# Kernel optimization log

Hardware: AMD Instinct MI355X
Metric: run time of the kernel (lower is better)

Reference implementation:

```python
import jax, jax.numpy as jnp
import numpy as np

NUM_NODES = 40000
NUM_EDGES = 400000
DIM = 128
NUM_REL = 502  # num_relation * 2
NUM_HEAD = 1


def setup_inputs() -> dict:
    key = jax.random.key(0)
    ks = jax.random.split(key, 16)
    d = DIM
    return {
        "curr_stat": jax.random.normal(ks[0], (NUM_NODES, d), jnp.float32),
        "last_stat": jax.random.normal(ks[1], (NUM_NODES, d), jnp.float32),
        "relemb_weight": jax.random.normal(ks[2], (NUM_REL, d), jnp.float32),
        "selfrel_weight": jax.random.normal(ks[3], (1, d), jnp.float32),
        "Wq": jax.random.normal(ks[4], (2 * d, d), jnp.float32) * (1.0 / np.sqrt(2 * d)),
        "bq": jax.random.normal(ks[5], (d,), jnp.float32) * 0.02,
        "Wk": jax.random.normal(ks[6], (2 * d, d), jnp.float32) * (1.0 / np.sqrt(2 * d)),
        "bk": jax.random.normal(ks[7], (d,), jnp.float32) * 0.02,
        "Wv": jax.random.normal(ks[8], (d, d), jnp.float32) * (1.0 / np.sqrt(d)),
        "bv": jax.random.normal(ks[9], (d,), jnp.float32) * 0.02,
        "dyn_weight": jax.random.normal(ks[10], (d, d), jnp.float32) * (1.0 / np.sqrt(d)),
        "edge_index": jax.random.randint(ks[11], (2, NUM_EDGES), 0, NUM_NODES, jnp.int32),
        "edge_type": jax.random.randint(ks[12], (NUM_EDGES,), 0, NUM_REL, jnp.int32),
    }


def _segment_softmax(scores, seg, num_segments):
    # scores: [E, H]; softmax over edges sharing the same destination segment
    m = jax.ops.segment_max(scores, seg, num_segments=num_segments)  # [N, H]
    e = jnp.exp(scores - m[seg])
    s = jax.ops.segment_sum(e, seg, num_segments=num_segments)  # [N, H]
    return e / s[seg]


def reference(curr_stat, last_stat, relemb_weight, selfrel_weight,
              Wq, bq, Wk, bk, Wv, bv, dyn_weight,
              edge_index, edge_type):
    N, D = curr_stat.shape
    H = NUM_HEAD
    HD = D // H

    # append self-loop edges for every node, with the dedicated self-relation
    loop = jnp.arange(N, dtype=edge_index.dtype)
    src = jnp.concatenate([edge_index[0], loop])  # [E_total]
    dst = jnp.concatenate([edge_index[1], loop])  # [E_total]
    type_emb = jnp.concatenate(
        [relemb_weight[edge_type], jnp.broadcast_to(selfrel_weight, (N, D))], axis=0)

    E = src.shape[0]
    # linear projections (x @ W + b); torch Linear stores W transposed, same math
    q = (jnp.concatenate([curr_stat[dst], type_emb], -1) @ Wq + bq).reshape(E, H, HD)
    k = (jnp.concatenate([last_stat[src], type_emb], -1) @ Wk + bk).reshape(E, H, HD)
    v = (last_stat[src] @ Wv + bv).reshape(E, H, HD)

    attn = jnp.sum(q * k, axis=-1) / np.sqrt(HD).astype(np.float32)  # [E, H]

    dyn_prob = _segment_softmax(attn, dst, N)   # [E, H]
    sta_prob = _segment_softmax(-attn, dst, N)  # [E, H]

    counts = jax.ops.segment_sum(jnp.ones((E,), jnp.float32), dst, num_segments=N)
    denom = jnp.maximum(counts, 1.0)[:, None]  # scatter-mean denominator

    feat_dyn = jax.ops.segment_sum((dyn_prob[..., None] * v).reshape(E, D), dst,
                                   num_segments=N) / denom
    feat_sta = jax.ops.segment_sum((sta_prob[..., None] * v).reshape(E, D), dst,
                                   num_segments=N) / denom

    # stack (feat_sta, feat_dyn @ dyn_weight) -> [2, N, D]
    return jnp.stack([feat_sta, feat_dyn @ dyn_weight])
```

## Files before the change

### kernel.cpp

```cpp
#include <hip/hip_runtime.h>
#include <hip/hip_bf16.h>
#include <math.h>

#define DIMC 128
#define CS2L (0.08838834764831845f * 1.4426950408889634f)

typedef __attribute__((ext_vector_type(8))) short short8;
typedef __attribute__((ext_vector_type(4))) float floatx4;
typedef __attribute__((ext_vector_type(2))) float f32x2;

static __device__ __forceinline__ unsigned pk2(float lo, float hi) {
    __hip_bfloat162 h = __float22bfloat162_rn(make_float2(lo, hi));
    return *(unsigned*)&h;
}
static __device__ __forceinline__ unsigned short f2bf(float x) {
    union { float f; unsigned int u; } v; v.f = x;
    unsigned int r = v.u + 0x7FFFu + ((v.u >> 16) & 1u);
    return (unsigned short)(r >> 16);
}
static __device__ __forceinline__ f32x2 bfp(unsigned int u) {
    union { unsigned int i; float f; } a, b;
    a.i = u << 16; b.i = u & 0xFFFF0000u;
    f32x2 r; r.x = a.f; r.y = b.f; return r;
}

template<int CTRL>
static __device__ __forceinline__ float dpp_add(float x) {
    int y = __builtin_amdgcn_update_dpp(0, __float_as_int(x), CTRL, 0xF, 0xF, true);
    return x + __int_as_float(y);
}
static __device__ __forceinline__ float red16(float p) {
    p = dpp_add<0xB1>(p);
    p = dpp_add<0x4E>(p);
    p = dpp_add<0x141>(p);
    p = dpp_add<0x140>(p);
    return p;
}

struct PrepArgs {
    const float* W[6];
    unsigned short* F[6];
    float wscale[6];
    const float* relemb; const float* selfrel;
    float* TypeEmb;
    int* deg;
    int R; int N;
};

__global__ __launch_bounds__(64) void prep_all(PrepArgs a)
{
    int b = blockIdx.x;
    int lane = threadIdx.x;
    if (b < 192) {
        int mat = b >> 5, ts = b & 31;
        int s = ts & 3, t = ts >> 2;
        int q = lane >> 4, c = lane & 15;
        const float* W = a.W[mat];
        float sc = a.wscale[mat];
        unsigned short o[8];
        #pragma unroll
        for (int j = 0; j < 8; ++j)
            o[j] = f2bf(W[(long)(s * 32 + q * 8 + j) * DIMC + t * 16 + c] * sc);
        uint4 u;
        u.x = (unsigned)o[0] | ((unsigned)o[1] << 16);
        u.y = (unsigned)o[2] | ((unsigned)o[3] << 16);
        u.z = (unsigned)o[4] | ((unsigned)o[5] << 16);
        u.w = (unsigned)o[6] | ((unsigned)o[7] << 16);
        ((uint4*)a.F[mat])[ts * 64 + lane] = u;
    } else if (b < 192 + a.R + 1) {
        int r = b - 192;
        const float* src = (r < a.R) ? (a.relemb + (long)r * DIMC) : a.selfrel;
        float2 v = ((const float2*)src)[lane];
        ((float2*)(a.TypeEmb + (long)r * DIMC))[lane] = v;
    } else {
        int i = (b - (192 + a.R + 1)) * 64 + lane;
        if (i < a.N) a.deg[i] = 0;
    }
}

struct GemmM5 {
    const float*          Af[5];
    const unsigned short* Ab[5];
    const unsigned short* F[5];
    const float*          bias[5];
    float                 bscale[5];
    float*                outf[5];
    unsigned short*       outb[5];
    int                   ostride[5];
    int                   ooff[5];
    int                   M[5];
    const unsigned short* F2;
    const float*          bias2;
    unsigned short*       outb2;
    const int*            hist_dst;
    int*                  hist_deg;
    int                   hist_E;
};

__global__ __launch_bounds__(256) void gemm_mfma(GemmM5 g)
{
    __shared__ uint4 wlds[2048];

    if (blockIdx.y == 4) {
        int i = blockIdx.x * blockDim.x + threadIdx.x;
        int stride = gridDim.x * blockDim.x;
        for (; i < g.hist_E; i += stride) atomicAdd(&g.hist_deg[g.hist_dst[i]], 1);
        return;
    }

    const int wave = threadIdx.x >> 6;
    const int lane = threadIdx.x & 63;
    const int q = lane >> 4, c = lane & 15;

    if (blockIdx.y == 1) {
        const int M = g.M[1];
        if ((int)blockIdx.x * 64 >= M) return;
        const int rowbase = blockIdx.x * 64 + wave * 16;

        {
            const uint4* Fp = (const uint4*)g.F[1];
            #pragma unroll
            for (int j = 0; j < 8; ++j)
                wlds[threadIdx.x + j * 256] = Fp[threadIdx.x + j * 256];
        }
        int rowA = rowbase + c; if (rowA > M - 1) rowA = M - 1;
        short8 af[4];
        {
            const float* Ar = g.Af[1] + (long)rowA * DIMC + q * 8;
            #pragma unroll
            for (int s = 0; s < 4; ++s) {
                float4 x0 = *(const float4*)(Ar + s * 32);
                float4 x1 = *(const float4*)(Ar + s * 32 + 4);
                uint4 u;
                u.x = pk2(x0.x, x0.y);
                u.y = pk2(x0.z, x0.w);
                u.z = pk2(x1.x, x1.y);
                u.w = pk2(x1.z, x1.w);
                af[s] = *(short8*)&u;
            }
        }
        floatx4 acc[8];
        #pragma unroll
        for (int t = 0; t < 8; ++t) acc[t] = (floatx4){0.f, 0.f, 0.f, 0.f};
        __syncthreads();
        #pragma unroll
        for (int t = 0; t < 8; ++t)
            #pragma unroll
            for (int s = 0; s < 4; ++s) {
                uint4 u = wlds[(t * 4 + s) * 64 + lane];
                acc[t] = __builtin_amdgcn_mfma_f32_16x16x32_bf16(af[s], *(short8*)&u, acc[t], 0, 0, 0);
            }
        __syncthreads();
        {
            const uint4* Fp = (const uint4*)g.F2;
            #pragma unroll
            for (int j = 0; j < 8; ++j)
                wlds[threadIdx.x + j * 256] = Fp[threadIdx.x + j * 256];
        }
        #pragma unroll
        for (int t = 0; t < 8; ++t)
            #pragma unroll
            for (int r = 0; r < 4; ++r) {
                float other = __shfl_xor(acc[t][r], 1);
                int row = rowbase + q * 4 + r;
                if ((lane & 1) == 0 && row < M)
                    ((unsigned*)g.outb[1])[(long)row * 64 + t * 8 + (c >> 1)] = pk2(acc[t][r], other);
            }
        #pragma unroll
        for (int t = 0; t < 8; ++t) {
            float b = g.bias2[t * 16 + c];
            acc[t] = (floatx4){b, b, b, b};
        }
        __syncthreads();
        #pragma unroll
        for (int t = 0; t < 8; ++t)
            #pragma unroll
            for (int s = 0; s < 4; ++s) {
                uint4 u = wlds[(t * 4 + s) * 64 + lane];
                acc[t] = __builtin_amdgcn_mfma_f32_16x16x32_bf16(af[s], *(short8*)&u, acc[t], 0, 0, 0);
            }
        #pragma unroll
        for (int t = 0; t < 8; ++t)
            #pragma unroll
            for (int r = 0; r < 4; ++r) {
                float other = __shfl_xor(acc[t][r], 1);
                int row = rowbase + q * 4 + r;
                if ((lane & 1) == 0 && row < M)
                    ((unsigned*)g.outb2)[(long)row * 64 + t * 8 + (c >> 1)] = pk2(acc[t][r], other);
            }
        return;
    }

    const int which = blockIdx.y;
    const int M = g.M[which];
    if ((int)blockIdx.x * 64 >= M) return;

    const float*          __restrict__ Af   = g.Af[which];
    const unsigned short* __restrict__ Ab   = g.Ab[which];
    const unsigned short* __restrict__ F    = g.F[which];
    const float*          __restrict__ bias = g.bias[which];
    const float bsc = g.bscale[which];
    float*          __restrict__ outf = g.outf[which];
    unsigned short* __restrict__ outb = g.outb[which];
    const int ostride = g.ostride[which];
    const int ooff    = g.ooff[which];
    const int rowbase = blockIdx.x * 64 + wave * 16;

    {
        const uint4* Fp = (const uint4*)F;
        #pragma unroll
        for (int j = 0; j < 8; ++j)
            wlds[threadIdx.x + j * 256] = Fp[threadIdx.x + j * 256];
    }

    int rowA = rowbase + c; if (rowA > M - 1) rowA = M - 1;
    short8 af[4];
    if (Af) {
        const float* Ar = Af + (long)rowA * DIMC + q * 8;
        #pragma unroll
        for (int s = 0; s < 4; ++s) {
            float4 x0 = *(const float4*)(Ar + s * 32);
            float4 x1 = *(const float4*)(Ar + s * 32 + 4);
            uint4 u;
            u.x = pk2(x0.x, x0.y);
            u.y = pk2(x0.z, x0.w);
            u.z = pk2(x1.x, x1.y);
            u.w = pk2(x1.z, x1.w);
            af[s] = *(short8*)&u;
        }
    } else {
        const unsigned short* Ar = Ab + (long)rowA * DIMC + q * 8;
        #pragma unroll
        for (int s = 0; s < 4; ++s) {
            uint4 u = *(const uint4*)(Ar + s * 32);
            af[s] = *(short8*)&u;
        }
    }

    floatx4 acc[8];
    #pragma unroll
    for (int t = 0; t < 8; ++t) {
        float b = bias ? bias[t * 16 + c] * bsc : 0.0f;
        acc[t] = (floatx4){b, b, b, b};
    }

    __syncthreads();

    #pragma unroll
    for (int t = 0; t < 8; ++t)
        #pragma unroll
        for (int s = 0; s < 4; ++s) {
            uint4 u = wlds[(t * 4 + s) * 64 + lane];
            acc[t] = __builtin_amdgcn_mfma_f32_16x16x32_bf16(af[s], *(short8*)&u, acc[t], 0, 0, 0);
        }

    if (outf) {
        #pragma unroll
        for (int t = 0; t < 8; ++t)
            #pragma unroll
            for (int r = 0; r < 4; ++r) {
                int row = rowbase + q * 4 + r;
                if (row < M)
                    outf[(long)row * DIMC + t * 16 + c] = acc[t][r];
            }
    } else {
        #pragma unroll
        for (int t = 0; t < 8; ++t)
            #pragma unroll
            for (int r = 0; r < 4; ++r) {
                float other = __shfl_xor(acc[t][r], 1);
                int row = rowbase + q * 4 + r;
                if ((lane & 1) == 0 && row < M) {
                    unsigned word = pk2(acc[t][r], other);
                    ((unsigned*)outb)[((long)row * 64 + t * 8 + (c >> 1))
                                      * (long)ostride + ooff] = word;
                }
            }
    }
}

__global__ __launch_bounds__(256) void partial_sums(const int* __restrict__ deg,
                                                    int* __restrict__ partial, int N)
{
    __shared__ int sh[256];
    int t = threadIdx.x;
    int beg = blockIdx.x * 1024 + t * 4;
    int s = 0;
    if (beg + 3 < N) { int4 v = *(const int4*)(deg + beg); s = v.x + v.y + v.z + v.w; }
    else { for (int j = 0; j < 4; ++j) if (beg + j < N) s += deg[beg + j]; }
    sh[t] = s;
    __syncthreads();
    for (int d = 128; d >= 1; d >>= 1) {
        if (t < d) sh[t] += sh[t + d];
        __syncthreads();
    }
    if (t == 0) partial[blockIdx.x] = sh[0];
}

__global__ __launch_bounds__(256) void scan_write_offsets(const int* __restrict__ deg,
                                                          const int* __restrict__ partial,
                                                          int* __restrict__ offs,
                                                          int* __restrict__ cursor, int N, int nb)
{
    __shared__ int sh[256];
    __shared__ int sbase;
    int t = threadIdx.x;
    if (t < 64) {
        int v = (t < nb && t < (int)blockIdx.x) ? partial[t] : 0;
        #pragma unroll
        for (int d = 32; d >= 1; d >>= 1) v += __shfl_xor(v, d);
        if (t == 0) sbase = v;
    }
    int beg = blockIdx.x * 1024 + t * 4;
    int d0 = 0, d1 = 0, d2 = 0, d3 = 0;
    if (beg + 3 < N) { int4 v = *(const int4*)(deg + beg); d0 = v.x; d1 = v.y; d2 = v.z; d3 = v.w; }
    else {
        if (beg < N)     d0 = deg[beg];
        if (beg + 1 < N) d1 = deg[beg + 1];
        if (beg + 2 < N) d2 = deg[beg + 2];
        if (beg + 3 < N) d3 = deg[beg + 3];
    }
    int s = d0 + d1 + d2 + d3;
    sh[t] = s;
    __syncthreads();
    for (int d = 1; d < 256; d <<= 1) {
        int v = (t >= d) ? sh[t - d] : 0;
        __syncthreads();
        sh[t] += v;
        __syncthreads();
    }
    int base = sbase + sh[t] - s;
    int o0 = base, o1 = o0 + d0, o2 = o1 + d1, o3 = o2 + d2;
    if (beg < N)     { offs[beg]     = o0; cursor[beg]     = o0; }
    if (beg + 1 < N) { offs[beg + 1] = o1; cursor[beg + 1] = o1; }
    if (beg + 2 < N) { offs[beg + 2] = o2; cursor[beg + 2] = o2; }
    if (beg + 3 < N) { offs[beg + 3] = o3; cursor[beg + 3] = o3; }
}

__global__ void scatter_kernel(const int* __restrict__ src, const int* __restrict__ dst,
                               const int* __restrict__ etype, int* __restrict__ cursor,
                               int2* __restrict__ sedge, int E)
{
    int e = blockIdx.x * blockDim.x + threadIdx.x;
    if (e < E) {
        int d = dst[e];
        int p = atomicAdd(&cursor[d], 1);
        sedge[p] = make_int2(src[e] << 8, etype[e] << 9);
    }
}

__global__ __launch_bounds__(256) void node_kernel(
    const char*  __restrict__ Qb,
    const char*  __restrict__ Kb,
    const char*  __restrict__ Vb,
    const char*  __restrict__ QKb,
    const int* __restrict__ offs, const int* __restrict__ deg,
    const int2* __restrict__ sedge,
    float* __restrict__ out_sta, uint2* __restrict__ feat_dyn,
    int N, int R)
{
    int n = (blockIdx.x * blockDim.x + threadIdx.x) >> 6;
    int lane = threadIdx.x & 63;
    if (n >= N) return;
    const int ql = lane & 31;
    const int h  = lane >> 5;
    const int lo8  = ql << 3;
    const int lo16 = ql << 4;

    int base = offs[n];
    int dcnt = deg[n];
    int etot = dcnt + 1;

    f32x2 q01, q23;
    {
        uint2 qw = *(const uint2*)(Qb + ((long)n << 8) + lo8);
        q01 = bfp(qw.x);
        q23 = bfp(qw.y);
    }

    float s_d = 0.0f, s_s = 0.0f;
    f32x2 accd0 = {0.f, 0.f}, accd1 = accd0;
    f32x2 accs0 = accd0, accs1 = accd0;

    const int selfK = n << 8, selfQ = R << 9;

    int T = (etot + 1) >> 1;
    for (int it = 0; it < T; ++it) {
        int i = 2 * it + h;
        bool vv = i < etot;
        bool re = i < dcnt;
        int2 e = re ? sedge[base + i] : make_int2(selfK, selfQ);

        uint2 kx  = *(const uint2*)(Kb + e.x + lo8);
        uint2 vx  = *(const uint2*)(Vb + e.x + lo8);
        uint4 qk  = *(const uint4*)(QKb + e.y + lo16);

        f32x2 a0 = q01 + bfp(qk.x), a1 = q23 + bfp(qk.z);
        f32x2 k0 = bfp(kx.x) + bfp(qk.y), k1 = bfp(kx.y) + bfp(qk.w);
        f32x2 dp = a0 * k0;
        dp += a1 * k1;
        float pd = dp.x + dp.y;
        pd = red16(pd);
        pd += __shfl_xor(pd, 16);

        float wd = vv ? exp2f(pd)  : 0.0f;
        float ws = vv ? exp2f(-pd) : 0.0f;
        s_d += wd; s_s += ws;

        f32x2 v0 = bfp(vx.x), v1 = bfp(vx.y);
        accd0 += v0 * wd; accd1 += v1 * wd;
        accs0 += v0 * ws; accs1 += v1 * ws;
    }

    s_d += __shfl_xor(s_d, 32);
    s_s += __shfl_xor(s_s, 32);
    accd0.x += __shfl_xor(accd0.x, 32); accd0.y += __shfl_xor(accd0.y, 32);
    accd1.x += __shfl_xor(accd1.x, 32); accd1.y += __shfl_xor(accd1.y, 32);
    accs0.x += __shfl_xor(accs0.x, 32); accs0.y += __shfl_xor(accs0.y, 32);
    accs1.x += __shfl_xor(accs1.x, 32); accs1.y += __shfl_xor(accs1.y, 32);

    if (h == 0) {
        float denom = (float)(dcnt + 1);
        float id_ = 1.0f / (s_d * denom);
        float is_ = 1.0f / (s_s * denom);
        ((float4*)(out_sta + (long)n * DIMC))[ql] =
            make_float4(accs0.x * is_, accs0.y * is_, accs1.x * is_, accs1.y * is_);
        feat_dyn[(unsigned)n * 32u + ql] =
            make_uint2(pk2(accd0.x * id_, accd0.y * id_), pk2(accd1.x * id_, accd1.y * id_));
    }
}

extern "C" void kernel_launch(void* const* d_in, const int* in_sizes, int n_in,
                              void* d_out, int out_size, void* d_ws, size_t ws_size,
                              hipStream_t stream)
{
    const float* curr    = (const float*)d_in[0];
    const float* last    = (const float*)d_in[1];
    const float* relemb  = (const float*)d_in[2];
    const float* selfrel = (const float*)d_in[3];
    const float* Wq      = (const float*)d_in[4];
    const float* bq      = (const float*)d_in[5];
    const float* Wk      = (const float*)d_in[6];
    const float* bk      = (const float*)d_in[7];
    const float* Wv      = (const float*)d_in[8];
    const float* bv      = (const float*)d_in[9];
    const float* dynw    = (const float*)d_in[10];
    const int*   eidx    = (const int*)d_in[11];
    const int*   etype   = (const int*)d_in[12];
    float* out = (float*)d_out;

    const int N = in_sizes[0] / DIMC;
    const int E = in_sizes[12];
    const int R = in_sizes[2] / DIMC;
    const int* esrc = eidx;
    const int* edst = eidx + E;

    char* wp = (char*)d_ws;
    auto alloc = [&](size_t bytes) { char* r = wp; wp += (bytes + 15) & ~(size_t)15; return r; };
    size_t nd = (size_t)N * DIMC;
    unsigned short* Qb    = (unsigned short*)alloc((size_t)N * 256);
    unsigned short* Kb    = (unsigned short*)alloc((size_t)N * 256);
    unsigned short* Vb    = (unsigned short*)alloc((size_t)N * 256);
    unsigned short* Fdb   = (unsigned short*)alloc(nd * 2);
    uint4*          QKre  = (uint4*)alloc((size_t)(R + 1) * 32 * 16);
    float*          TypeEmb = (float*)alloc((size_t)(R + 2) * DIMC * 4);
    unsigned short* FW[6];
    for (int m = 0; m < 6; ++m) FW[m] = (unsigned short*)alloc(2048 * 8 * 2);
    int*            deg   = (int*)alloc((size_t)N * 4);
    int*            offs  = (int*)alloc((size_t)N * 4);
    int*            cursor= (int*)alloc((size_t)N * 4);
    int2*           sedge = (int2*)alloc((size_t)E * 8);
    int*            partial = (int*)alloc(256 * 4);

    const int gblk = N / 64;
    const int sblk = (N + 1023) / 1024;

    PrepArgs pa;
    pa.W[0] = Wq;   pa.W[1] = Wk;   pa.W[2] = Wv;
    pa.W[3] = dynw; pa.W[4] = Wq + (size_t)DIMC * DIMC; pa.W[5] = Wk + (size_t)DIMC * DIMC;
    pa.wscale[0] = CS2L; pa.wscale[1] = 1.0f; pa.wscale[2] = 1.0f;
    pa.wscale[3] = 1.0f; pa.wscale[4] = CS2L; pa.wscale[5] = 1.0f;
    for (int m = 0; m < 6; ++m) pa.F[m] = FW[m];
    pa.relemb = relemb; pa.selfrel = selfrel; pa.TypeEmb = TypeEmb;
    pa.deg = deg; pa.R = R; pa.N = N;
    int pgrid = 192 + (R + 1) + (N + 63) / 64;
    hipLaunchKernelGGL(prep_all, dim3(pgrid), dim3(64), 0, stream, pa);

    GemmM5 g5;
    for (int s = 0; s < 5; ++s) { g5.Af[s] = nullptr; g5.Ab[s] = nullptr; g5.outf[s] = nullptr; g5.outb[s] = nullptr; g5.bias[s] = nullptr; g5.bscale[s] = 1.0f; g5.ostride[s] = 1; g5.ooff[s] = 0; g5.M[s] = 0; }
    g5.Af[0] = curr;    g5.F[0] = FW[0]; g5.outb[0] = Qb;  g5.M[0] = N;
    g5.Af[1] = last;    g5.F[1] = FW[1]; g5.outb[1] = Kb;  g5.M[1] = N;
    g5.F2 = FW[2]; g5.bias2 = bv; g5.outb2 = Vb;
    g5.Af[2] = TypeEmb; g5.F[2] = FW[4]; g5.bias[2] = bq;  g5.outb[2] = (unsigned short*)QKre;
    g5.ostride[2] = 2;  g5.ooff[2] = 0;  g5.M[2] = R + 1;  g5.bscale[2] = CS2L;
    g5.Af[3] = TypeEmb; g5.F[3] = FW[5]; g5.bias[3] = bk;  g5.outb[3] = (unsigned short*)QKre;
    g5.ostride[3] = 2;  g5.ooff[3] = 1;  g5.M[3] = R + 1;
    g5.hist_dst = edst; g5.hist_deg = deg; g5.hist_E = E;
    hipLaunchKernelGGL(gemm_mfma, dim3(gblk, 5), dim3(256), 0, stream, g5);

    hipLaunchKernelGGL(partial_sums, dim3(sblk), dim3(256), 0, stream, deg, partial, N);
    hipLaunchKernelGGL(scan_write_offsets, dim3(sblk), dim3(256), 0, stream,
                       deg, partial, offs, cursor, N, sblk);
    hipLaunchKernelGGL(scatter_kernel, dim3((E + 255) / 256), dim3(256), 0, stream,
                       esrc, edst, etype, cursor, sedge, E);

    hipLaunchKernelGGL(node_kernel, dim3((N + 3) / 4), dim3(256), 0, stream,
                       (const char*)Qb, (const char*)Kb, (const char*)Vb, (const char*)QKre,
                       offs, deg, sedge, out, (uint2*)Fdb, N, R);

    GemmM5 gf;
    for (int s = 0; s < 5; ++s) { gf.Af[s] = nullptr; gf.Ab[s] = nullptr; gf.outf[s] = nullptr; gf.outb[s] = nullptr; gf.bias[s] = nullptr; gf.bscale[s] = 1.0f; gf.ostride[s] = 1; gf.ooff[s] = 0; gf.M[s] = 0; }
    gf.Ab[0] = Fdb; gf.F[0] = FW[3]; gf.outf[0] = out + nd; gf.M[0] = N;
    gf.F2 = FW[2]; gf.bias2 = bv; gf.outb2 = Vb;
    gf.hist_dst = edst; gf.hist_deg = deg; gf.hist_E = 0;
    hipLaunchKernelGGL(gemm_mfma, dim3(gblk, 1), dim3(256), 0, stream, gf);
}
```

Before: 215.4 us.

## Process four edges per wavefront with 16-lane groups and prefetch edge indices

The node kernel now splits each 64-lane wavefront into four 16-lane groups, each handling a different edge and loading 16-byte vectors of K, V and the relation terms per lane, instead of two 32-lane groups with 8-byte loads. The next edge descriptor is loaded one iteration ahead to hide the index-load latency. This halves the per-edge reduction depth and doubles edge-level parallelism, in exchange for more accumulator registers and a two-stage cross-group shuffle merge at the end. Nodes with few edges may leave more lane groups idle.

```diff
diff --git a/kernel.cpp b/kernel.cpp
--- a/kernel.cpp
+++ b/kernel.cpp
@@ -356,77 +356,93 @@
     const char*  __restrict__ QKb,
     const int* __restrict__ offs, const int* __restrict__ deg,
     const int2* __restrict__ sedge,
-    float* __restrict__ out_sta, uint2* __restrict__ feat_dyn,
+    float* __restrict__ out_sta, uint4* __restrict__ feat_dyn,
     int N, int R)
 {
     int n = (blockIdx.x * blockDim.x + threadIdx.x) >> 6;
     int lane = threadIdx.x & 63;
     if (n >= N) return;
-    const int ql = lane & 31;
-    const int h  = lane >> 5;
-    const int lo8  = ql << 3;
+    const int ql = lane & 15;
+    const int qt = lane >> 4;
     const int lo16 = ql << 4;
+    const int lo32 = ql << 5;
 
     int base = offs[n];
     int dcnt = deg[n];
     int etot = dcnt + 1;
 
-    f32x2 q01, q23;
+    f32x2 qr0, qr1, qr2, qr3;
     {
-        uint2 qw = *(const uint2*)(Qb + ((long)n << 8) + lo8);
-        q01 = bfp(qw.x);
-        q23 = bfp(qw.y);
+        uint4 qw = *(const uint4*)(Qb + ((long)n << 8) + lo16);
+        qr0 = bfp(qw.x); qr1 = bfp(qw.y); qr2 = bfp(qw.z); qr3 = bfp(qw.w);
     }
 
     float s_d = 0.0f, s_s = 0.0f;
-    f32x2 accd0 = {0.f, 0.f}, accd1 = accd0;
-    f32x2 accs0 = accd0, accs1 = accd0;
-
-    const int selfK = n << 8, selfQ = R << 9;
-
-    int T = (etot + 1) >> 1;
+    f32x2 accd0 = {0.f, 0.f}, accd1 = accd0, accd2 = accd0, accd3 = accd0;
+    f32x2 accs0 = accd0, accs1 = accd0, accs2 = accd0, accs3 = accd0;
+
+    const int2 eself = make_int2(n << 8, R << 9);
+
+    int T = (etot + 3) >> 2;
+    int2 eCur = eself;
+    {
+        int i = qt;
+        if (i < dcnt) eCur = sedge[base + i];
+    }
     for (int it = 0; it < T; ++it) {
-        int i = 2 * it + h;
+        int i = 4 * it + qt;
         bool vv = i < etot;
-        bool re = i < dcnt;
-        int2 e = re ? sedge[base + i] : make_int2(selfK, selfQ);
-
-        uint2 kx  = *(const uint2*)(Kb + e.x + lo8);
-        uint2 vx  = *(const uint2*)(Vb + e.x + lo8);
-        uint4 qk  = *(const uint4*)(QKb + e.y + lo16);
-
-        f32x2 a0 = q01 + bfp(qk.x), a1 = q23 + bfp(qk.z);
-        f32x2 k0 = bfp(kx.x) + bfp(qk.y), k1 = bfp(kx.y) + bfp(qk.w);
-        f32x2 dp = a0 * k0;
-        dp += a1 * k1;
-        float pd = dp.x + dp.y;
-        pd = red16(pd);
-        pd += __shfl_xor(pd, 16);
-
-        float wd = vv ? exp2f(pd)  : 0.0f;
-        float ws = vv ? exp2f(-pd) : 0.0f;
+
+        int2 eNxt = eself;
+        if (it + 1 < T) {
+            int inx = 4 * (it + 1) + qt;
+            if (inx < dcnt) eNxt = sedge[base + inx];
+        }
+
+        uint4 kx  = *(const uint4*)(Kb + eCur.x + lo16);
+        uint4 vx  = *(const uint4*)(Vb + eCur.x + lo16);
+        uint4 qk0 = *(const uint4*)(QKb + eCur.y + lo32);
+        uint4 qk1 = *(const uint4*)(QKb + eCur.y + lo32 + 16);
+
+        f32x2 dp;
+        dp  = (qr0 + bfp(qk0.x)) * (bfp(kx.x) + bfp(qk0.y));
+        dp += (qr1 + bfp(qk0.z)) * (bfp(kx.y) + bfp(qk0.w));
+        dp += (qr2 + bfp(qk1.x)) * (bfp(kx.z) + bfp(qk1.y));
+        dp += (qr3 + bfp(qk1.z)) * (bfp(kx.w) + bfp(qk1.w));
+        float p = red16(dp.x + dp.y);
+
+        float wd = vv ? exp2f(p)  : 0.0f;
+        float ws = vv ? exp2f(-p) : 0.0f;
         s_d += wd; s_s += ws;
 
-        f32x2 v0 = bfp(vx.x), v1 = bfp(vx.y);
-        accd0 += v0 * wd; accd1 += v1 * wd;
-        accs0 += v0 * ws; accs1 += v1 * ws;
-    }
-
-    s_d += __shfl_xor(s_d, 32);
-    s_s += __shfl_xor(s_s, 32);
-    accd0.x += __shfl_xor(accd0.x, 32); accd0.y += __shfl_xor(accd0.y, 32);
-    accd1.x += __shfl_xor(accd1.x, 32); accd1.y += __shfl_xor(accd1.y, 32);
-    accs0.x += __shfl_xor(accs0.x, 32); accs0.y += __shfl_xor(accs0.y, 32);
-    accs1.x += __shfl_xor(accs1.x, 32); accs1.y += __shfl_xor(accs1.y, 32);
-
-    if (h == 0) {
+        f32x2 v0 = bfp(vx.x), v1 = bfp(vx.y), v2 = bfp(vx.z), v3 = bfp(vx.w);
+        accd0 += v0 * wd; accd1 += v1 * wd; accd2 += v2 * wd; accd3 += v3 * wd;
+        accs0 += v0 * ws; accs1 += v1 * ws; accs2 += v2 * ws; accs3 += v3 * ws;
+
+        eCur = eNxt;
+    }
+
+    #define MRG(x) { x += __shfl_xor(x, 16); x += __shfl_xor(x, 32); }
+    MRG(s_d) MRG(s_s)
+    MRG(accd0.x) MRG(accd0.y) MRG(accd1.x) MRG(accd1.y)
+    MRG(accd2.x) MRG(accd2.y) MRG(accd3.x) MRG(accd3.y)
+    MRG(accs0.x) MRG(accs0.y) MRG(accs1.x) MRG(accs1.y)
+    MRG(accs2.x) MRG(accs2.y) MRG(accs3.x) MRG(accs3.y)
+    #undef MRG
+
+    if (qt == 0) {
         float denom = (float)(dcnt + 1);
         float id_ = 1.0f / (s_d * denom);
         float is_ = 1.0f / (s_s * denom);
-        ((float4*)(out_sta + (long)n * DIMC))[ql] =
-            make_float4(accs0.x * is_, accs0.y * is_, accs1.x * is_, accs1.y * is_);
-        feat_dyn[(unsigned)n * 32u + ql] =
-            make_uint2(pk2(accd0.x * id_, accd0.y * id_), pk2(accd1.x * id_, accd1.y * id_));
+        float4* op = (float4*)(out_sta + (long)n * DIMC + ql * 8);
+        op[0] = make_float4(accs0.x * is_, accs0.y * is_, accs1.x * is_, accs1.y * is_);
+        op[1] = make_float4(accs2.x * is_, accs2.y * is_, accs3.x * is_, accs3.y * is_);
+        uint4 w;
+        w.x = pk2(accd0.x * id_, accd0.y * id_);
+        w.y = pk2(accd1.x * id_, accd1.y * id_);
+        w.z = pk2(accd2.x * id_, accd2.y * id_);
+        w.w = pk2(accd3.x * id_, accd3.y * id_);
+        feat_dyn[(unsigned)n * 16u + ql] = w;
     }
 }
 
@@ -506,7 +522,7 @@
 
     hipLaunchKernelGGL(node_kernel, dim3((N + 3) / 4), dim3(256), 0, stream,
                        (const char*)Qb, (const char*)Kb, (const char*)Vb, (const char*)QKre,
-                       offs, deg, sedge, out, (uint2*)Fdb, N, R);
+                       offs, deg, sedge, out, (uint4*)Fdb, N, R);
 
     GemmM5 gf;
     for (int s = 0; s < 5; ++s) { gf.Af[s] = nullptr; gf.Ab[s] = nullptr; gf.outf[s] = nullptr; gf.outb[s] = nullptr; gf.bias[s] = nullptr; gf.bscale[s] = 1.0f; gf.ostride[s] = 1; gf.ooff[s] = 0; gf.M[s] = 0; }
```

New measurement: 209.7 us (median of 3 runs). -2.6%, faster.
